# Kernel optimization log

Hardware: AMD Instinct MI355X
Metric: run time of the kernel (lower is better)

## Reference

```python
import jax, jax.numpy as jnp
import numpy as np


def setup_inputs() -> dict:
    key = jax.random.key(0)
    ks = jax.random.split(key, 8)
    B, C, H, W = 4, 128, 128, 128
    C8 = C // 8
    x = jax.random.normal(ks[0], (B, C, H, W), jnp.float32)
    # 1x1 conv weights as [out, in] matrices + biases
    Wq = jax.random.normal(ks[1], (C8, C), jnp.float32) * 0.05
    bq = jax.random.normal(ks[2], (C8,), jnp.float32) * 0.01
    Wk = jax.random.normal(ks[3], (C8, C), jnp.float32) * 0.05
    bk = jax.random.normal(ks[4], (C8,), jnp.float32) * 0.01
    Wv = jax.random.normal(ks[5], (C, C), jnp.float32) * 0.05
    bv = jax.random.normal(ks[6], (C,), jnp.float32) * 0.01
    # nn.Parameter(torch.zeros(1)) in the original; use nonzero so output/grads are nontrivial
    gamma = jax.random.normal(ks[7], (), jnp.float32) * 0.1
    return {"x": x, "Wq": Wq, "bq": bq, "Wk": Wk, "bk": bk,
            "Wv": Wv, "bv": bv, "gamma": gamma}


def reference(x, Wq, bq, Wk, bk, Wv, bv, gamma):
    # x: [b, c, h, w]
    b, c, h, w = x.shape
    # 1x1 convs == channel contractions
    q = jnp.einsum('bchw,oc->bohw', x, Wq) + bq[None, :, None, None]  # [b,c8,h,w]
    k = jnp.einsum('bchw,oc->bohw', x, Wk) + bk[None, :, None, None]  # [b,c8,h,w]
    v = jnp.einsum('bchw,oc->bohw', x, Wv) + bv[None, :, None, None]  # [b,c, h,w]

    # column (height) attention logits: e_h[b, h1, w, h2], diagonal masked to -inf
    e_h = jnp.einsum('bcxw,bcyw->bxwy', q, k)
    diag = jnp.eye(h, dtype=bool)  # [h1, h2]
    e_h = jnp.where(diag[:, None, :], -jnp.inf, e_h)
    # row (width) attention logits: e_w[b, h, w1, w2]
    e_w = jnp.einsum('bchx,bchy->bhxy', q, k)

    # joint softmax over concatenated (h2 + w2) axis
    attn = jax.nn.softmax(jnp.concatenate([e_h, e_w], axis=3), axis=3)  # [b,h,w,h+w]
    attn_h = attn[..., :h]   # [b, h1, w, h2]
    attn_w = attn[..., h:]   # [b, h, w1, w2]

    # aggregate values along columns and rows
    out_h = jnp.einsum('bcyw,bxwy->bcxw', v, attn_h)  # [b,c,h,w]
    out_w = jnp.einsum('bchy,bhxy->bchx', v, attn_w)  # [b,c,h,w]

    out = gamma * (out_h + out_w) + x
    # return_attn: stack([b h2 h1 w, b w2 h w1], dim=1)
    return_attn = jnp.stack([jnp.transpose(attn_h, (0, 3, 1, 2)),
                             jnp.transpose(attn_w, (0, 3, 1, 2))], axis=1)
    return out, return_attn
```

## Files before the change

### kernel.cpp

```cpp
#include <hip/hip_runtime.h>
#include <math.h>

#define HW_ 16384
#define SLOT_ 2097152ULL
#define BSTR_ 4194304ULL

typedef __attribute__((ext_vector_type(8))) short short8v;
typedef __attribute__((ext_vector_type(4))) float f32x4;

__device__ __forceinline__ unsigned short f2bf(float f) {
  unsigned int u = __float_as_uint(f);
  u = (u + 0x7FFFu + ((u >> 16) & 1u)) >> 16;
  return (unsigned short)u;
}
__device__ __forceinline__ float bf2f(unsigned short h) {
  return __uint_as_float(((unsigned int)h) << 16);
}

__global__ void __launch_bounds__(256, 2)
qkv_proj(const float* __restrict__ x,
         const float* __restrict__ Wq, const float* __restrict__ bq,
         const float* __restrict__ Wk, const float* __restrict__ bk,
         const float* __restrict__ Wv, const float* __restrict__ bv,
         float* __restrict__ qT, float* __restrict__ kT,
         unsigned short* __restrict__ vA0,
         unsigned short* __restrict__ Ew, float* __restrict__ rsw) {
  __shared__ float WT[128][36];
  __shared__ float BUF[8448];
  float (*Wc)[132] = (float(*)[132])BUF;
  float (*Xc)[132] = (float(*)[132])(BUF + 4224);
  int t = threadIdx.x;
  for (int i = t; i < 4096; i += 256) {
    int o = i >> 7, c = i & 127;
    WT[c][o] = (o < 16) ? Wq[o * 128 + c] : Wk[(o - 16) * 128 + c];
  }
  int blk = blockIdx.x;
  int b = blk >> 7, h = blk & 127;
  int p0 = h * 128;
  int tc = t & 15, tx = t >> 4;
  float acc[8][8];
#pragma unroll
  for (int ci = 0; ci < 8; ++ci) {
    float bvv = bv[tc * 8 + ci];
#pragma unroll
    for (int pi = 0; pi < 8; ++pi) acc[ci][pi] = bvv;
  }
  float accqk[2][8];
#pragma unroll
  for (int e = 0; e < 2; ++e) {
    int och = tc * 2 + e;
    float bias = (och < 16) ? bq[och] : bk[och - 16];
#pragma unroll
    for (int pi = 0; pi < 8; ++pi) accqk[e][pi] = bias;
  }
  int c2 = t >> 1, part = t & 1;
  const float* xb = x + (size_t)b * 128 * HW_ + p0;
  float4 pw[4], px[4];
#pragma unroll
  for (int qq = 0; qq < 4; ++qq)
    pw[qq] = *(const float4*)&Wv[c2 * 128 + part * 16 + qq * 4];
#pragma unroll
  for (int r = 0; r < 4; ++r) {
    int idx = r * 1024 + t * 4;
    px[r] = *(const float4*)&xb[(size_t)(idx >> 7) * HW_ + (idx & 127)];
  }
  __syncthreads();
  for (int k0 = 0; k0 < 128; k0 += 32) {
#pragma unroll
    for (int qq = 0; qq < 4; ++qq) {
      int y4 = part * 16 + qq * 4;
      Wc[y4 + 0][c2] = pw[qq].x;
      Wc[y4 + 1][c2] = pw[qq].y;
      Wc[y4 + 2][c2] = pw[qq].z;
      Wc[y4 + 3][c2] = pw[qq].w;
    }
#pragma unroll
    for (int r = 0; r < 4; ++r) {
      int idx = r * 1024 + t * 4;
      *(float4*)&Xc[idx >> 7][idx & 127] = px[r];
    }
    __syncthreads();
    if (k0 < 96) {
#pragma unroll
      for (int qq = 0; qq < 4; ++qq)
        pw[qq] = *(const float4*)&Wv[c2 * 128 + (k0 + 32) + part * 16 + qq * 4];
#pragma unroll
      for (int r = 0; r < 4; ++r) {
        int idx = r * 1024 + t * 4;
        px[r] = *(const float4*)&xb[(size_t)(k0 + 32 + (idx >> 7)) * HW_ + (idx & 127)];
      }
    }
    for (int kl = 0; kl < 32; ++kl) {
      float wa[8], xa[8];
      *(float4*)(wa)     = *(const float4*)&Wc[kl][tc * 8];
      *(float4*)(wa + 4) = *(const float4*)&Wc[kl][tc * 8 + 4];
      *(float4*)(xa)     = *(const float4*)&Xc[kl][tx * 8];
      *(float4*)(xa + 4) = *(const float4*)&Xc[kl][tx * 8 + 4];
      float wq0 = WT[k0 + kl][tc * 2];
      float wq1 = WT[k0 + kl][tc * 2 + 1];
#pragma unroll
      for (int ci = 0; ci < 8; ++ci)
#pragma unroll
        for (int pi = 0; pi < 8; ++pi)
          acc[ci][pi] = fmaf(wa[ci], xa[pi], acc[ci][pi]);
#pragma unroll
      for (int pi = 0; pi < 8; ++pi) {
        accqk[0][pi] = fmaf(wq0, xa[pi], accqk[0][pi]);
        accqk[1][pi] = fmaf(wq1, xa[pi], accqk[1][pi]);
      }
    }
    __syncthreads();
  }
#pragma unroll
  for (int ci = 0; ci < 8; ++ci) {
    union { unsigned short us[8]; uint4 v; } pk;
#pragma unroll
    for (int pi = 0; pi < 8; ++pi) pk.us[pi] = f2bf(acc[ci][pi]);
    *(uint4*)&vA0[(size_t)(b * 128 + h) * 16384 + (size_t)(tc * 8 + ci) * 128 + tx * 8] = pk.v;
  }
  float (*QKs)[36] = (float(*)[36])BUF;
#pragma unroll
  for (int e = 0; e < 2; ++e)
#pragma unroll
    for (int pi = 0; pi < 8; ++pi)
      QKs[tx * 8 + pi][tc * 2 + e] = accqk[e][pi];
  __syncthreads();
  {
    int px_ = t >> 1, sel = t & 1;
    const float* qr = &QKs[px_][sel * 16];
    float4 r0 = *(const float4*)(qr);
    float4 r1 = *(const float4*)(qr + 4);
    float4 r2 = *(const float4*)(qr + 8);
    float4 r3 = *(const float4*)(qr + 12);
    float* dstT = (sel ? kT : qT) + ((size_t)(b * HW_ + px_ * 128 + h)) * 16;
    *(float4*)(dstT)      = r0;
    *(float4*)(dstT + 4)  = r1;
    *(float4*)(dstT + 8)  = r2;
    *(float4*)(dstT + 12) = r3;
  }
  float (*Qs)[132] = (float(*)[132])&WT[0][0];
  float (*Ks)[132] = (float(*)[132])(&WT[0][0] + 2112);
  {
    int cc = t & 15, pb = (t >> 4) * 8;
#pragma unroll
    for (int u = 0; u < 8; ++u) {
      Qs[cc][pb + u] = QKs[pb + u][cc];
      Ks[cc][pb + u] = QKs[pb + u][16 + cc];
    }
  }
  __syncthreads();
  {
    int tr = (t >> 4) * 8;
    int ty = (t & 15) * 8;
    float sc_[8][8] = {{0.f}};
#pragma unroll
    for (int c = 0; c < 16; ++c) {
      float qa[8], ka[8];
      *(float4*)(qa)     = *(const float4*)&Qs[c][tr];
      *(float4*)(qa + 4) = *(const float4*)&Qs[c][tr + 4];
      *(float4*)(ka)     = *(const float4*)&Ks[c][ty];
      *(float4*)(ka + 4) = *(const float4*)&Ks[c][ty + 4];
#pragma unroll
      for (int u = 0; u < 8; ++u)
#pragma unroll
        for (int v = 0; v < 8; ++v)
          sc_[u][v] = fmaf(qa[u], ka[v], sc_[u][v]);
    }
    float rp[8];
#pragma unroll
    for (int u = 0; u < 8; ++u) {
      rp[u] = 0.f;
#pragma unroll
      for (int v = 0; v < 8; ++v) {
        float e = __expf(sc_[u][v]);
        sc_[u][v] = e;
        rp[u] += e;
      }
    }
    unsigned short* out = Ew + (size_t)blk * 16384;
#pragma unroll
    for (int u = 0; u < 8; ++u) {
      union { unsigned short us[8]; uint4 v; } pk;
#pragma unroll
      for (int v = 0; v < 8; ++v) pk.us[v] = f2bf(sc_[u][v]);
      *(uint4*)&out[(tr + u) * 128 + ty] = pk.v;
    }
#pragma unroll
    for (int u = 0; u < 8; ++u) {
      rp[u] += __shfl_xor(rp[u], 1);
      rp[u] += __shfl_xor(rp[u], 2);
      rp[u] += __shfl_xor(rp[u], 4);
      rp[u] += __shfl_xor(rp[u], 8);
    }
    if ((t & 15) == 0) {
#pragma unroll
      for (int u = 0; u < 8; ++u) rsw[(size_t)blk * 128 + tr + u] = rp[u];
    }
  }
}

__global__ void score_h(const float* __restrict__ Q, const float* __restrict__ K,
                        unsigned short* __restrict__ E, float* __restrict__ rsum,
                        size_t ebs, size_t eoff) {
  __shared__ float Qs[16][132];
  __shared__ float Ks[16][132];
  int slab = blockIdx.x;
  int b = slab >> 7, s = slab & 127;
  const float* qb = Q + (size_t)slab * 2048;
  const float* kb = K + (size_t)slab * 2048;
  int t = threadIdx.x;
  int cc = t & 15;
  int pb = (t >> 4) * 8;
#pragma unroll
  for (int u = 0; u < 8; ++u) {
    Qs[cc][pb + u] = qb[(size_t)(pb + u) * 16 + cc];
    Ks[cc][pb + u] = kb[(size_t)(pb + u) * 16 + cc];
  }
  __syncthreads();
  int tr = (t >> 4) * 8;
  int ty = (t & 15) * 8;
  float acc[8][8] = {{0.f}};
#pragma unroll
  for (int c = 0; c < 16; ++c) {
    float qa[8], ka[8];
    *(float4*)(qa)     = *(const float4*)&Qs[c][tr];
    *(float4*)(qa + 4) = *(const float4*)&Qs[c][tr + 4];
    *(float4*)(ka)     = *(const float4*)&Ks[c][ty];
    *(float4*)(ka + 4) = *(const float4*)&Ks[c][ty + 4];
#pragma unroll
    for (int u = 0; u < 8; ++u)
#pragma unroll
      for (int v = 0; v < 8; ++v)
        acc[u][v] = fmaf(qa[u], ka[v], acc[u][v]);
  }
  float rp[8];
#pragma unroll
  for (int u = 0; u < 8; ++u) {
    rp[u] = 0.f;
#pragma unroll
    for (int v = 0; v < 8; ++v) {
      float e = __expf(acc[u][v]);
      if ((tr + u) == (ty + v)) e = 0.f;
      acc[u][v] = e;
      rp[u] += e;
    }
  }
  unsigned short* out = E + (size_t)b * ebs + eoff + (size_t)s * 16384;
#pragma unroll
  for (int u = 0; u < 8; ++u) {
    union { unsigned short us[8]; uint4 v; } pk;
#pragma unroll
    for (int v = 0; v < 8; ++v) pk.us[v] = f2bf(acc[u][v]);
    *(uint4*)&out[(tr + u) * 128 + ty] = pk.v;
  }
#pragma unroll
  for (int u = 0; u < 8; ++u) {
    rp[u] += __shfl_xor(rp[u], 1);
    rp[u] += __shfl_xor(rp[u], 2);
    rp[u] += __shfl_xor(rp[u], 4);
    rp[u] += __shfl_xor(rp[u], 8);
  }
  if ((t & 15) == 0) {
#pragma unroll
    for (int u = 0; u < 8; ++u) rsum[(size_t)slab * 128 + tr + u] = rp[u];
  }
}

__global__ void trans_v(const unsigned short* __restrict__ vA0, unsigned short* __restrict__ vA1,
                        const float* __restrict__ rsw, const float* __restrict__ rsh,
                        float* __restrict__ dij, float* __restrict__ dji) {
  __shared__ unsigned short tile[64][65];
  int blk = blockIdx.x;
  int q = blk & 3, c = (blk >> 2) & 127, b = blk >> 9;
  int h0 = (q >> 1) * 64, w0 = (q & 1) * 64;
  int t = threadIdx.x, lane = t & 63, r0 = (t >> 6) * 16;
  for (int r = r0; r < r0 + 16; ++r)
    tile[r][lane] = vA0[(size_t)(b * 128 + h0 + r) * 16384 + c * 128 + w0 + lane];
  __syncthreads();
  for (int r = r0; r < r0 + 16; ++r)
    vA1[(size_t)(b * 128 + w0 + r) * 16384 + c * 128 + h0 + lane] = tile[lane][r];
  if (blk < 256) {
    int p = blk * 256 + t;
    int bb = p >> 14, rem = p & 16383, i = rem >> 7, j = rem & 127;
    float d = rsw[p] + rsh[(size_t)bb * HW_ + j * 128 + i];
    float r = 1.0f / d;
    dij[p] = r;
    dji[(size_t)bb * HW_ + j * 128 + i] = r;
  }
}

__global__ void pv2(const unsigned short* __restrict__ vA0,
                    const unsigned short* __restrict__ vA1,
                    const unsigned short* __restrict__ Ew,
                    const unsigned short* __restrict__ EhB,
                    const float* __restrict__ dij, const float* __restrict__ dji,
                    unsigned short* __restrict__ ow, unsigned short* __restrict__ ohb) {
  __shared__ unsigned short Al[128][44];
  __shared__ unsigned short Bl[128][44];
  int blk = blockIdx.x;
  int m = blk >> 9;
  int slab = blk & 511;
  int s = slab & 127, b = slab >> 7;
  int t = threadIdx.x;
  int wv = t >> 6, l = t & 63;
  int wc = (wv >> 1) * 64, wx = (wv & 1) * 64;
  const unsigned short* vs = (m ? vA1 : vA0) + (size_t)slab * 16384;
  const unsigned short* es = m ? (EhB + (size_t)b * 8388608 + 4194304 + (size_t)s * 16384)
                               : (Ew + (size_t)slab * 16384);
  const float* invd = m ? dji : dij;
  f32x4 acc[4][4];
#pragma unroll
  for (int mi = 0; mi < 4; ++mi)
#pragma unroll
    for (int ni = 0; ni < 4; ++ni) acc[mi][ni] = (f32x4){0.f, 0.f, 0.f, 0.f};
  int lrow = t >> 2, lq = t & 3;
  int lm = l & 15, lk = (l >> 4) * 4;
  for (int y0 = 0; y0 < 128; y0 += 32) {
#pragma unroll
    for (int r = 0; r < 2; ++r) {
      int rr = lrow + r * 64;
      uint4 av = *(const uint4*)(vs + (size_t)rr * 128 + y0 + lq * 8);
      uint4 bv = *(const uint4*)(es + (size_t)rr * 128 + y0 + lq * 8);
      *(uint2*)&Al[rr][lq * 8]     = make_uint2(av.x, av.y);
      *(uint2*)&Al[rr][lq * 8 + 4] = make_uint2(av.z, av.w);
      *(uint2*)&Bl[rr][lq * 8]     = make_uint2(bv.x, bv.y);
      *(uint2*)&Bl[rr][lq * 8 + 4] = make_uint2(bv.z, bv.w);
    }
    __syncthreads();
    short8v af[4], bf[4];
#pragma unroll
    for (int mi = 0; mi < 4; ++mi) {
      const unsigned short* ap = &Al[wc + mi * 16 + lm][lk];
      union { uint2 p[2]; short8v v; } u;
      u.p[0] = *(const uint2*)ap;
      u.p[1] = *(const uint2*)(ap + 16);
      af[mi] = u.v;
    }
#pragma unroll
    for (int ni = 0; ni < 4; ++ni) {
      const unsigned short* bp = &Bl[wx + ni * 16 + lm][lk];
      union { uint2 p[2]; short8v v; } u;
      u.p[0] = *(const uint2*)bp;
      u.p[1] = *(const uint2*)(bp + 16);
      bf[ni] = u.v;
    }
#pragma unroll
    for (int mi = 0; mi < 4; ++mi)
#pragma unroll
      for (int ni = 0; ni < 4; ++ni)
        acc[mi][ni] = __builtin_amdgcn_mfma_f32_16x16x32_bf16(af[mi], bf[ni], acc[mi][ni], 0, 0, 0);
    __syncthreads();
  }
  int lr4 = (l >> 4) * 4;
  unsigned short* dst = m ? ohb : ow;
#pragma unroll
  for (int ni = 0; ni < 4; ++ni) {
    int xx = wx + ni * 16 + lm;
    float idv = invd[(size_t)(b * 128 + s) * 128 + xx];
#pragma unroll
    for (int mi = 0; mi < 4; ++mi) {
#pragma unroll
      for (int r = 0; r < 4; ++r) {
        int c = wc + mi * 16 + lr4 + r;
        size_t idx = m ? ((size_t)b * 8388608 + (size_t)s * 16384 + (size_t)c * 128 + xx)
                       : ((((size_t)(b * 128 + c)) * 128 + s) * 128 + xx);
        dst[idx] = f2bf(acc[mi][ni][r] * idv);
      }
    }
  }
}

__global__ void merge2(const unsigned short* __restrict__ ow,
                       const unsigned short* __restrict__ ohp,
                       const float* __restrict__ xin, const float* __restrict__ gamma,
                       float* __restrict__ outp) {
  __shared__ float tile[64][65];
  int blk = blockIdx.x;
  int q = blk & 3, c = (blk >> 2) & 127, b = blk >> 9;
  int h0 = (q >> 1) * 64, w0 = (q & 1) * 64;
  int t = threadIdx.x, lane = t & 63, r0 = (t >> 6) * 16;
  for (int r = r0; r < r0 + 16; ++r)
    tile[r][lane] =
        bf2f(ohp[(size_t)b * 8388608ULL + (size_t)(w0 + r) * 16384 + c * 128 + h0 + lane]);
  __syncthreads();
  float g = gamma[0];
  for (int r = r0; r < r0 + 16; ++r) {
    size_t a = (((size_t)(b * 128 + c)) * 128 + h0 + r) * 128 + w0 + lane;
    outp[a] = g * (bf2f(ow[a]) + tile[lane][r]) + xin[a];
  }
}

template <int HM>
__global__ void ret_write(const unsigned short* __restrict__ src, const float* __restrict__ invd,
                          float* __restrict__ retb, size_t sbs, size_t soff) {
  __shared__ float tile[128][129];
  __shared__ float idv[128];
  int slab = blockIdx.x;
  int b = slab >> 7, i = slab & 127;
  int t = threadIdx.x;
  const unsigned short* sp = src + (size_t)b * sbs + soff;
#pragma unroll
  for (int r = 0; r < 8; ++r) {
    int idx = r * 2048 + t * 8;
    int j = idx >> 7, y = idx & 127;
    uint4 raw;
    if (HM == 0)
      raw = *(const uint4*)(sp + (size_t)i * 16384 + j * 128 + y);
    else
      raw = *(const uint4*)(sp + (size_t)j * 16384 + i * 128 + y);
    unsigned int wd[4] = {raw.x, raw.y, raw.z, raw.w};
#pragma unroll
    for (int e = 0; e < 4; ++e) {
      tile[j][y + 2 * e]     = __uint_as_float((wd[e] & 0xFFFFu) << 16);
      tile[j][y + 2 * e + 1] = __uint_as_float(wd[e] & 0xFFFF0000u);
    }
  }
  if (t < 128) idv[t] = invd[(size_t)slab * 128 + t];
  __syncthreads();
  float* dp = retb + (size_t)b * BSTR_ + (HM == 0 ? SLOT_ : 0);
#pragma unroll
  for (int r = 0; r < 16; ++r) {
    int idx = r * 1024 + t * 4;
    int y = idx >> 7, j = idx & 127;
    float4 o;
    o.x = tile[j][y]     * idv[j];
    o.y = tile[j + 1][y] * idv[j + 1];
    o.z = tile[j + 2][y] * idv[j + 2];
    o.w = tile[j + 3][y] * idv[j + 3];
    *(float4*)&dp[(size_t)y * 16384 + i * 128 + j] = o;
  }
}

extern "C" void kernel_launch(void* const* d_in, const int* in_sizes, int n_in,
                              void* d_out, int out_size, void* d_ws, size_t ws_size,
                              hipStream_t stream) {
  const float* x     = (const float*)d_in[0];
  const float* Wq    = (const float*)d_in[1];
  const float* bq    = (const float*)d_in[2];
  const float* Wk    = (const float*)d_in[3];
  const float* bk    = (const float*)d_in[4];
  const float* Wv    = (const float*)d_in[5];
  const float* bv    = (const float*)d_in[6];
  const float* gamma = (const float*)d_in[7];

  float* outp = (float*)d_out;
  float* retb = outp + (size_t)8388608;
  unsigned short* ohb = (unsigned short*)retb;
  unsigned short* ehb = (unsigned short*)retb;

  float* ws      = (float*)d_ws;
  float* qT      = ws + (size_t)2097152;
  float* kT      = ws + (size_t)3145728;
  unsigned short* ow  = (unsigned short*)ws;
  unsigned short* vA0 = (unsigned short*)(ws + (size_t)4194304);
  unsigned short* vA1 = (unsigned short*)(ws + (size_t)8388608);
  unsigned short* E_w = (unsigned short*)(ws + (size_t)12582912);
  float* rsum_w  = ws + (size_t)16777216;
  float* rsum_h  = ws + (size_t)16842752;
  float* invd_ij = ws + (size_t)16908288;
  float* invd_ji = ws + (size_t)16973824;

  qkv_proj<<<512, 256, 0, stream>>>(x, Wq, bq, Wk, bk, Wv, bv,
                                    qT, kT, vA0, E_w, rsum_w);
  score_h<<<512, 256, 0, stream>>>(qT, kT, ehb, rsum_h,
                                   (size_t)8388608, (size_t)4194304);
  trans_v<<<2048, 256, 0, stream>>>(vA0, vA1, rsum_w, rsum_h, invd_ij, invd_ji);
  pv2<<<1024, 256, 0, stream>>>(vA0, vA1, E_w, ehb, invd_ij, invd_ji, ow, ohb);
  merge2<<<2048, 256, 0, stream>>>(ow, ohb, x, gamma, outp);
  ret_write<1><<<512, 256, 0, stream>>>(ehb, invd_ij, retb, (size_t)8388608, (size_t)4194304);
  ret_write<0><<<512, 256, 0, stream>>>(E_w, invd_ij, retb, (size_t)2097152, (size_t)0);
}
```

Measured before the change: 139.3 us.

## Compute QKV projection with bf16 MFMA instead of fp32 FMA loops

Replaces the scalar fp32 register-tiled GEMM in the QKV projection kernel with bf16 MFMA 16x16x32 instructions. Weights and the input tile are converted to bf16 and staged in LDS, with x transposed. The Q/K projection now runs at bf16 input precision, which adds rounding error to the attention logits. The x transpose uses scalar strided LDS writes and the vA0 stores are now per-element, so the load and store side may be less efficient.

```diff
diff --git a/kernel.cpp b/kernel.cpp
--- a/kernel.cpp
+++ b/kernel.cpp
@@ -25,105 +25,119 @@
          float* __restrict__ qT, float* __restrict__ kT,
          unsigned short* __restrict__ vA0,
          unsigned short* __restrict__ Ew, float* __restrict__ rsw) {
-  __shared__ float WT[128][36];
-  __shared__ float BUF[8448];
-  float (*Wc)[132] = (float(*)[132])BUF;
-  float (*Xc)[132] = (float(*)[132])(BUF + 4224);
+  __shared__ unsigned short LDSU[39168];
+  unsigned short (*WqkL)[136] = (unsigned short(*)[136])LDSU;
+  unsigned short (*WvL)[136]  = (unsigned short(*)[136])(LDSU + 4352);
+  unsigned short (*XT)[136]   = (unsigned short(*)[136])(LDSU + 21760);
   int t = threadIdx.x;
-  for (int i = t; i < 4096; i += 256) {
-    int o = i >> 7, c = i & 127;
-    WT[c][o] = (o < 16) ? Wq[o * 128 + c] : Wk[(o - 16) * 128 + c];
-  }
   int blk = blockIdx.x;
   int b = blk >> 7, h = blk & 127;
-  int p0 = h * 128;
-  int tc = t & 15, tx = t >> 4;
-  float acc[8][8];
-#pragma unroll
-  for (int ci = 0; ci < 8; ++ci) {
-    float bvv = bv[tc * 8 + ci];
-#pragma unroll
-    for (int pi = 0; pi < 8; ++pi) acc[ci][pi] = bvv;
-  }
-  float accqk[2][8];
-#pragma unroll
-  for (int e = 0; e < 2; ++e) {
-    int och = tc * 2 + e;
-    float bias = (och < 16) ? bq[och] : bk[och - 16];
-#pragma unroll
-    for (int pi = 0; pi < 8; ++pi) accqk[e][pi] = bias;
-  }
-  int c2 = t >> 1, part = t & 1;
-  const float* xb = x + (size_t)b * 128 * HW_ + p0;
-  float4 pw[4], px[4];
-#pragma unroll
-  for (int qq = 0; qq < 4; ++qq)
-    pw[qq] = *(const float4*)&Wv[c2 * 128 + part * 16 + qq * 4];
+  {
+    int och = t >> 3, kb = (t & 7) * 16;
+    const float* src = (och < 16 ? Wq + och * 128 : Wk + (och - 16) * 128) + kb;
+    union { unsigned short us[8]; uint4 v; } p0, p1;
+#pragma unroll
+    for (int j = 0; j < 8; ++j) p0.us[j] = f2bf(src[j]);
+#pragma unroll
+    for (int j = 0; j < 8; ++j) p1.us[j] = f2bf(src[8 + j]);
+    *(uint4*)&WqkL[och][kb]     = p0.v;
+    *(uint4*)&WqkL[och][kb + 8] = p1.v;
+  }
+  {
+    int c = t >> 1, kb = (t & 1) * 64;
+    const float* src = Wv + c * 128 + kb;
+#pragma unroll
+    for (int g = 0; g < 8; ++g) {
+      union { unsigned short us[8]; uint4 v; } p;
+#pragma unroll
+      for (int j = 0; j < 8; ++j) p.us[j] = f2bf(src[g * 8 + j]);
+      *(uint4*)&WvL[c][kb + g * 8] = p.v;
+    }
+  }
+  {
+    int k = t >> 1, pxb = (t & 1) * 64;
+    const float* src = x + (size_t)b * 128 * HW_ + (size_t)k * HW_ + h * 128 + pxb;
+#pragma unroll
+    for (int j = 0; j < 64; ++j)
+      XT[pxb + j][k] = f2bf(src[j]);
+  }
+  int wv = t >> 6, l = t & 63;
+  int lm = l & 15, lk = (l >> 4) * 4, lr4 = (l >> 4) * 4;
+  int wc = (wv >> 1) * 64, wx = (wv & 1) * 64;
+  int ocht = (wv >> 1) * 16;
+  float bvr[4][4];
+#pragma unroll
+  for (int mi = 0; mi < 4; ++mi)
+#pragma unroll
+    for (int r = 0; r < 4; ++r) bvr[mi][r] = bv[wc + mi * 16 + lr4 + r];
+  float bqk[4];
 #pragma unroll
   for (int r = 0; r < 4; ++r) {
-    int idx = r * 1024 + t * 4;
-    px[r] = *(const float4*)&xb[(size_t)(idx >> 7) * HW_ + (idx & 127)];
-  }
-  __syncthreads();
-  for (int k0 = 0; k0 < 128; k0 += 32) {
-#pragma unroll
-    for (int qq = 0; qq < 4; ++qq) {
-      int y4 = part * 16 + qq * 4;
-      Wc[y4 + 0][c2] = pw[qq].x;
-      Wc[y4 + 1][c2] = pw[qq].y;
-      Wc[y4 + 2][c2] = pw[qq].z;
-      Wc[y4 + 3][c2] = pw[qq].w;
-    }
-#pragma unroll
-    for (int r = 0; r < 4; ++r) {
-      int idx = r * 1024 + t * 4;
-      *(float4*)&Xc[idx >> 7][idx & 127] = px[r];
-    }
-    __syncthreads();
-    if (k0 < 96) {
-#pragma unroll
-      for (int qq = 0; qq < 4; ++qq)
-        pw[qq] = *(const float4*)&Wv[c2 * 128 + (k0 + 32) + part * 16 + qq * 4];
+    int och = ocht + lr4 + r;
+    bqk[r] = (och < 16) ? bq[och] : bk[och - 16];
+  }
+  f32x4 acc[4][4];
+#pragma unroll
+  for (int mi = 0; mi < 4; ++mi)
+#pragma unroll
+    for (int ni = 0; ni < 4; ++ni) acc[mi][ni] = (f32x4){0.f, 0.f, 0.f, 0.f};
+  f32x4 acc2[4];
+#pragma unroll
+  for (int ni = 0; ni < 4; ++ni) acc2[ni] = (f32x4){0.f, 0.f, 0.f, 0.f};
+  __syncthreads();
+  for (int y0 = 0; y0 < 128; y0 += 32) {
+    short8v bf[4];
+#pragma unroll
+    for (int ni = 0; ni < 4; ++ni) {
+      const unsigned short* bp = &XT[wx + ni * 16 + lm][y0 + lk];
+      union { uint2 p[2]; short8v v; } u;
+      u.p[0] = *(const uint2*)bp;
+      u.p[1] = *(const uint2*)(bp + 16);
+      bf[ni] = u.v;
+    }
+#pragma unroll
+    for (int mi = 0; mi < 4; ++mi) {
+      const unsigned short* ap = &WvL[wc + mi * 16 + lm][y0 + lk];
+      union { uint2 p[2]; short8v v; } u;
+      u.p[0] = *(const uint2*)ap;
+      u.p[1] = *(const uint2*)(ap + 16);
+      short8v af = u.v;
+#pragma unroll
+      for (int ni = 0; ni < 4; ++ni)
+        acc[mi][ni] = __builtin_amdgcn_mfma_f32_16x16x32_bf16(af, bf[ni], acc[mi][ni], 0, 0, 0);
+    }
+    {
+      const unsigned short* ap = &WqkL[ocht + lm][y0 + lk];
+      union { uint2 p[2]; short8v v; } u;
+      u.p[0] = *(const uint2*)ap;
+      u.p[1] = *(const uint2*)(ap + 16);
+      short8v aq = u.v;
+#pragma unroll
+      for (int ni = 0; ni < 4; ++ni)
+        acc2[ni] = __builtin_amdgcn_mfma_f32_16x16x32_bf16(aq, bf[ni], acc2[ni], 0, 0, 0);
+    }
+  }
+#pragma unroll
+  for (int ni = 0; ni < 4; ++ni) {
+    int px = wx + ni * 16 + lm;
+#pragma unroll
+    for (int mi = 0; mi < 4; ++mi)
 #pragma unroll
       for (int r = 0; r < 4; ++r) {
-        int idx = r * 1024 + t * 4;
-        px[r] = *(const float4*)&xb[(size_t)(k0 + 32 + (idx >> 7)) * HW_ + (idx & 127)];
+        int c = wc + mi * 16 + lr4 + r;
+        vA0[(size_t)(b * 128 + h) * 16384 + (size_t)c * 128 + px] =
+            f2bf(acc[mi][ni][r] + bvr[mi][r]);
       }
-    }
-    for (int kl = 0; kl < 32; ++kl) {
-      float wa[8], xa[8];
-      *(float4*)(wa)     = *(const float4*)&Wc[kl][tc * 8];
-      *(float4*)(wa + 4) = *(const float4*)&Wc[kl][tc * 8 + 4];
-      *(float4*)(xa)     = *(const float4*)&Xc[kl][tx * 8];
-      *(float4*)(xa + 4) = *(const float4*)&Xc[kl][tx * 8 + 4];
-      float wq0 = WT[k0 + kl][tc * 2];
-      float wq1 = WT[k0 + kl][tc * 2 + 1];
-#pragma unroll
-      for (int ci = 0; ci < 8; ++ci)
-#pragma unroll
-        for (int pi = 0; pi < 8; ++pi)
-          acc[ci][pi] = fmaf(wa[ci], xa[pi], acc[ci][pi]);
-#pragma unroll
-      for (int pi = 0; pi < 8; ++pi) {
-        accqk[0][pi] = fmaf(wq0, xa[pi], accqk[0][pi]);
-        accqk[1][pi] = fmaf(wq1, xa[pi], accqk[1][pi]);
-      }
-    }
-    __syncthreads();
-  }
-#pragma unroll
-  for (int ci = 0; ci < 8; ++ci) {
-    union { unsigned short us[8]; uint4 v; } pk;
-#pragma unroll
-    for (int pi = 0; pi < 8; ++pi) pk.us[pi] = f2bf(acc[ci][pi]);
-    *(uint4*)&vA0[(size_t)(b * 128 + h) * 16384 + (size_t)(tc * 8 + ci) * 128 + tx * 8] = pk.v;
-  }
-  float (*QKs)[36] = (float(*)[36])BUF;
-#pragma unroll
-  for (int e = 0; e < 2; ++e)
-#pragma unroll
-    for (int pi = 0; pi < 8; ++pi)
-      QKs[tx * 8 + pi][tc * 2 + e] = accqk[e][pi];
+  }
+  __syncthreads();
+  float (*QKs)[36] = (float(*)[36])(LDSU + 21760);
+#pragma unroll
+  for (int ni = 0; ni < 4; ++ni) {
+    int px = (wv & 1) * 64 + ni * 16 + lm;
+#pragma unroll
+    for (int r = 0; r < 4; ++r)
+      QKs[px][ocht + lr4 + r] = acc2[ni][r] + bqk[r];
+  }
   __syncthreads();
   {
     int px_ = t >> 1, sel = t & 1;
@@ -138,8 +152,8 @@
     *(float4*)(dstT + 8)  = r2;
     *(float4*)(dstT + 12) = r3;
   }
-  float (*Qs)[132] = (float(*)[132])&WT[0][0];
-  float (*Ks)[132] = (float(*)[132])(&WT[0][0] + 2112);
+  float (*Qs)[132] = (float(*)[132])(LDSU + 4352);
+  float (*Ks)[132] = (float(*)[132])(LDSU + 8576);
   {
     int cc = t & 15, pb = (t >> 4) * 8;
 #pragma unroll
```

Measured after the change: 111.7 us. 19.8% less time.
